# Kernel tuning notes

Hardware: AMD Instinct MI355X
Metric: run time of the kernel (lower is better)

The kernel has to match this reference:

```python
import jax, jax.numpy as jnp
import numpy as np

N_SITES = 64   # lattice sites
BOND = 32      # virtual bond dimension D
PHYS = 2       # physical (spin) dimension
BATCH = 32768  # Monte Carlo samples


def spin_to_occupancy(s):
    # spins in {-1,+1} -> physical indices in {0,1}
    return ((s + 1) // 2).astype(jnp.int32)


def setup_inputs() -> dict:
    key = jax.random.key(0)
    k1, k2, k3, k4 = jax.random.split(key, 4)
    # site tensors: boundary sites have bond dim 1, interior sites are (PHYS, D, D)
    t_first = jax.random.uniform(k1, (PHYS, 1, BOND), dtype=jnp.float32)
    t_mid = jax.random.uniform(k2, (N_SITES - 2, PHYS, BOND, BOND), dtype=jnp.float32)
    t_last = jax.random.uniform(k3, (PHYS, BOND, 1), dtype=jnp.float32)
    bits = jax.random.randint(k4, (BATCH, N_SITES), 0, 2)
    x = (2 * bits - 1).astype(jnp.int32)  # spins +-1
    return {"t_first": t_first, "t_mid": t_mid, "t_last": t_last, "x": x}


def reference(t_first, t_mid, t_last, x):
    idx = spin_to_occupancy(x)  # (B, n_sites)
    # first site: left bond = 1, so state = t_first[idx0, 0, :]  (B, D)
    state = t_first[idx[:, 0], 0, :]

    # interior sites: sequential chain of gather + batched mat-vec
    def step(state, xs):
        T, i = xs            # T: (PHYS, D, D), i: (B,)
        mats = T[i]          # (B, D, D) gather by physical index
        return jnp.einsum('bi,bij->bj', state, mats), None

    state, _ = jax.lax.scan(step, state, (t_mid, idx[:, 1:-1].T))

    # last site: right bond = 1
    amps = jnp.einsum('bi,bi->b', state, t_last[idx[:, -1], :, 0])  # (B,)
    return jnp.log(amps)
```

## Files before the change

kernel.cpp:

```cpp
#include <hip/hip_runtime.h>
#include <math.h>

#define NPAIR 31
#define BATCH 32768

typedef float f32x4 __attribute__((ext_vector_type(4)));
typedef int   i32x8 __attribute__((ext_vector_type(8)));
typedef unsigned int u32x2 __attribute__((ext_vector_type(2)));
typedef unsigned int u32x4 __attribute__((ext_vector_type(4)));

__device__ __forceinline__ unsigned pack_fp8x4(float a, float b, float c, float d) {
    int r = __builtin_amdgcn_cvt_pk_fp8_f32(a, b, 0, false);
    r = __builtin_amdgcn_cvt_pk_fp8_f32(c, d, r, true);
    return (unsigned)r;
}

__device__ __forceinline__ void lane_swap16(unsigned a, unsigned& ev, unsigned& od) {
#if __has_builtin(__builtin_amdgcn_permlane16_swap)
    auto r = __builtin_amdgcn_permlane16_swap((int)a, (int)a, false, false);
    ev = (unsigned)r[0]; od = (unsigned)r[1];
#else
    unsigned p = (unsigned)__shfl_xor((int)a, 16);
    bool hi = (threadIdx.x >> 4) & 1;
    ev = hi ? p : a; od = hi ? a : p;
#endif
}
__device__ __forceinline__ void lane_swap32(unsigned a, unsigned& lo, unsigned& hi) {
#if __has_builtin(__builtin_amdgcn_permlane32_swap)
    auto r = __builtin_amdgcn_permlane32_swap((int)a, (int)a, false, false);
    lo = (unsigned)r[0]; hi = (unsigned)r[1];
#else
    unsigned p = (unsigned)__shfl_xor((int)a, 32);
    bool up = (threadIdx.x & 32) != 0;
    lo = up ? p : a; hi = up ? a : p;
#endif
}

__global__ __launch_bounds__(64) void prefix_kernel(const float* __restrict__ t_mid,
                                                    unsigned* __restrict__ wsP) {
    __shared__ float M1s[1024], M2s[1024];
    const int l = threadIdx.x, h = l >> 4, m = l & 15;
    const int i = blockIdx.x >> 2, v = blockIdx.x & 3;

    const float4* s1 = (const float4*)(t_mid + (size_t)((2 * i) * 2 + (v & 1)) * 1024);
    const float4* s2 = (const float4*)(t_mid + (size_t)((2 * i + 1) * 2 + (v >> 1)) * 1024);
    #pragma unroll
    for (int c = 0; c < 4; ++c) {
        ((float4*)M1s)[c * 64 + l] = s1[c * 64 + l];
        ((float4*)M2s)[c * 64 + l] = s2[c * 64 + l];
    }
    __syncthreads();

    float colv[2][32];
    #pragma unroll
    for (int t = 0; t < 2; ++t)
        #pragma unroll
        for (int mm = 0; mm < 32; ++mm)
            colv[t][mm] = M2s[mm * 32 + 16 * t + m];

    float o0[8], o1[8];
    #pragma unroll
    for (int j = 0; j < 8; ++j) {
        int a = 16 * (j >> 2) + 4 * h + (j & 3);
        float acc0 = 0.f, acc1 = 0.f;
        #pragma unroll
        for (int mm = 0; mm < 32; ++mm) {
            float r = M1s[a * 32 + mm];
            acc0 = fmaf(r, colv[0][mm], acc0);
            acc1 = fmaf(r, colv[1][mm], acc1);
        }
        o0[j] = acc0;
        o1[j] = acc1;
    }

    unsigned* dst0 = wsP + (((size_t)blockIdx.x * 2 + 0) * 16 + m) * 8 + h * 2;
    u32x2 w0 = {pack_fp8x4(o0[0], o0[1], o0[2], o0[3]),
                pack_fp8x4(o0[4], o0[5], o0[6], o0[7])};
    *(u32x2*)dst0 = w0;
    unsigned* dst1 = wsP + (((size_t)blockIdx.x * 2 + 1) * 16 + m) * 8 + h * 2;
    u32x2 w1 = {pack_fp8x4(o1[0], o1[1], o1[2], o1[3]),
                pack_fp8x4(o1[4], o1[5], o1[6], o1[7])};
    *(u32x2*)dst1 = w1;
}

#define MPS_STEP(QQ, PF) do {                                                 \
    unsigned vl = (unsigned)mrot & 3u; mrot >>= 2;                            \
    unsigned E0, O0, E1, O1;                                                  \
    lane_swap16(Bd0, E0, O0); lane_swap16(Bd1, E1, O1);                       \
    unsigned g0, g1, g2, g3, g4, g5, g6, g7;                                  \
    lane_swap32(E0, g0, g4); lane_swap32(E1, g1, g5);                         \
    lane_swap32(O0, g2, g6); lane_swap32(O1, g3, g7);                         \
    bool selq = (vl == (unsigned)q);                                          \
    i32x8 Bv;                                                                 \
    Bv[0] = selq ? (int)g0 : 0; Bv[1] = selq ? (int)g1 : 0;                   \
    Bv[2] = selq ? (int)g2 : 0; Bv[3] = selq ? (int)g3 : 0;                   \
    Bv[4] = selq ? (int)g4 : 0; Bv[5] = selq ? (int)g5 : 0;                   \
    Bv[6] = selq ? (int)g6 : 0; Bv[7] = selq ? (int)g7 : 0;                   \
    i32x8 A0v, A1v;                                                           \
    A0v[0]=(int)QQ[0][0]; A0v[1]=(int)QQ[0][1]; A0v[2]=(int)QQ[0][2]; A0v[3]=(int)QQ[0][3]; \
    A0v[4]=(int)QQ[1][0]; A0v[5]=(int)QQ[1][1]; A0v[6]=(int)QQ[1][2]; A0v[7]=(int)QQ[1][3]; \
    A1v[0]=(int)QQ[2][0]; A1v[1]=(int)QQ[2][1]; A1v[2]=(int)QQ[2][2]; A1v[3]=(int)QQ[2][3]; \
    A1v[4]=(int)QQ[3][0]; A1v[5]=(int)QQ[3][1]; A1v[6]=(int)QQ[3][2]; A1v[7]=(int)QQ[3][3]; \
    const u32x4* pf_ = (PF);                                                  \
    if (pf_) { QQ[0] = pf_[0]; QQ[1] = pf_[1]; QQ[2] = pf_[32]; QQ[3] = pf_[33]; } \
    f32x4 y0 = __builtin_amdgcn_mfma_scale_f32_16x16x128_f8f6f4(              \
        A0v, Bv, cz, 0, 0, 0, 0x7f7f7f7f, 0, 0x7f7f7f7f);                     \
    f32x4 y1 = __builtin_amdgcn_mfma_scale_f32_16x16x128_f8f6f4(              \
        A1v, Bv, cz, 0, 0, 0, 0x7f7f7f7f, 0, 0x7f7f7f7f);                     \
    _Pragma("unroll")                                                         \
    for (int r = 0; r < 4; ++r) { st[r] = y0[r]; st[4 + r] = y1[r]; }         \
    float mx = fmaxf(fmaxf(fmaxf(st[0], st[1]), fmaxf(st[2], st[3])),         \
                     fmaxf(fmaxf(st[4], st[5]), fmaxf(st[6], st[7])));        \
    { unsigned a_, b_;                                                        \
      lane_swap16(__float_as_uint(mx), a_, b_);                               \
      mx = fmaxf(__uint_as_float(a_), __uint_as_float(b_));                   \
      lane_swap32(__float_as_uint(mx), a_, b_);                               \
      mx = fmaxf(__uint_as_float(a_), __uint_as_float(b_)); }                 \
    int ex = (int)((__float_as_uint(mx) >> 23) & 0xFF) - 127;                 \
    float sc = __uint_as_float((unsigned)(127 - ex) << 23);                   \
    _Pragma("unroll")                                                         \
    for (int j = 0; j < 8; ++j) st[j] *= sc;                                  \
    expsum += ex;                                                             \
    Bd0 = pack_fp8x4(st[0], st[1], st[2], st[3]);                             \
    Bd1 = pack_fp8x4(st[4], st[5], st[6], st[7]);                             \
} while (0)

__global__ __launch_bounds__(256, 2) void mps_mfma_kernel(
    const float* __restrict__ t_first,
    const float* __restrict__ t_last,
    const int*   __restrict__ x,
    const unsigned* __restrict__ wsP,
    float* __restrict__ out)
{
    const int tid  = threadIdx.x;
    const int w    = tid >> 6;
    const int l    = tid & 63;
    const int q    = l >> 4;
    const int e    = l & 15;
    const int base = (blockIdx.x * 4 + w) * 16;

    unsigned long long mrot;
    {
        const int4* xr = (const int4*)(x + (size_t)(base + e) * 64 + 16 * q);
        unsigned chunk = 0;
        #pragma unroll
        for (int c = 0; c < 4; ++c) {
            int4 vv = xr[c];
            chunk |= (unsigned)(vv.x > 0) << (4 * c + 0);
            chunk |= (unsigned)(vv.y > 0) << (4 * c + 1);
            chunk |= (unsigned)(vv.z > 0) << (4 * c + 2);
            chunk |= (unsigned)(vv.w > 0) << (4 * c + 3);
        }
        unsigned sh = chunk << ((q & 1) * 16);
        unsigned lo = (q < 2) ? sh : 0u;
        unsigned hi = (q >= 2) ? sh : 0u;
        lo |= (unsigned)__shfl_xor((int)lo, 16);
        lo |= (unsigned)__shfl_xor((int)lo, 32);
        hi |= (unsigned)__shfl_xor((int)hi, 16);
        hi |= (unsigned)__shfl_xor((int)hi, 32);
        unsigned long long mask = ((unsigned long long)hi << 32) | lo;
        mrot = mask >> 1;
    }

    float st[8];
    {
        const float* tf = t_first + ((x[(size_t)(base + e) * 64] > 0) ? 32 : 0);
        #pragma unroll
        for (int j = 0; j < 8; ++j)
            st[j] = tf[16 * (j >> 2) + 4 * q + (j & 3)];
    }
    unsigned Bd0 = pack_fp8x4(st[0], st[1], st[2], st[3]);
    unsigned Bd1 = pack_fp8x4(st[4], st[5], st[6], st[7]);

    int expsum = 0;
    const f32x4 cz = {0.f, 0.f, 0.f, 0.f};

    const u32x4* Wl = (const u32x4*)wsP + (q * 64 + e * 2);
    u32x4 Q0[4], Q1[4];
    Q0[0] = Wl[0];   Q0[1] = Wl[1];   Q0[2] = Wl[32];  Q0[3] = Wl[33];
    Q1[0] = Wl[256]; Q1[1] = Wl[257]; Q1[2] = Wl[288]; Q1[3] = Wl[289];

    const u32x4* pf = Wl + 512;
    for (int k = 0; k < 15; ++k) {
        MPS_STEP(Q0, pf);
        MPS_STEP(Q1, (k < 14) ? (pf + 256) : (const u32x4*)0);
        pf += 512;
    }
    MPS_STEP(Q0, (const u32x4*)0);

    const float* tl = t_last + ((mrot & 1ull) ? 32 : 0);
    float amp = 0.f;
    #pragma unroll
    for (int j = 0; j < 8; ++j)
        amp = fmaf(st[j], tl[16 * (j >> 2) + 4 * q + (j & 3)], amp);
    amp += __shfl_xor(amp, 16);
    amp += __shfl_xor(amp, 32);

    if (l < 16)
        out[base + l] = logf(amp) + 0.69314718055994531f * (float)expsum;
}

extern "C" void kernel_launch(void* const* d_in, const int* in_sizes, int n_in,
                              void* d_out, int out_size, void* d_ws, size_t ws_size,
                              hipStream_t stream) {
    const float* t_first = (const float*)d_in[0];
    const float* t_mid   = (const float*)d_in[1];
    const float* t_last  = (const float*)d_in[2];
    const int*   x       = (const int*)d_in[3];
    float* out           = (float*)d_out;

    unsigned* wsP = (unsigned*)d_ws;

    hipLaunchKernelGGL(prefix_kernel, dim3(NPAIR * 4), dim3(64), 0, stream, t_mid, wsP);
    hipLaunchKernelGGL(mps_mfma_kernel, dim3(BATCH / 64), dim3(256), 0, stream,
                       t_first, t_last, x, wsP, out);
}
```

Baseline: 80.64 us.

## Relayout fp8 pair-product workspace for coalesced loads and deepen prefetch to two steps

The precompute kernel now writes the packed fp8 pair matrices so that each lane's A-fragment for a step sits in contiguous 64-lane rows. The main kernel can then load it with fully coalesced 16-byte loads indexed by lane. The chain loop is fully unrolled with a 4-slot register ring that prefetches two steps ahead instead of one, to hide global load latency behind the MFMA and rescale chain. This costs more VGPRs, which could pressure the 2-waves-per-SIMD launch bound.

```diff
diff --git a/kernel.cpp b/kernel.cpp
--- a/kernel.cpp
+++ b/kernel.cpp
@@ -73,57 +73,16 @@
         o1[j] = acc1;
     }
 
-    unsigned* dst0 = wsP + (((size_t)blockIdx.x * 2 + 0) * 16 + m) * 8 + h * 2;
+    const int slot4 = (v * 16 + m) * 4 + (h & 1) * 2;
+    unsigned* dst0 = wsP + (size_t)(4 * i + (h >> 1)) * 256 + slot4;
     u32x2 w0 = {pack_fp8x4(o0[0], o0[1], o0[2], o0[3]),
                 pack_fp8x4(o0[4], o0[5], o0[6], o0[7])};
     *(u32x2*)dst0 = w0;
-    unsigned* dst1 = wsP + (((size_t)blockIdx.x * 2 + 1) * 16 + m) * 8 + h * 2;
+    unsigned* dst1 = wsP + (size_t)(4 * i + 2 + (h >> 1)) * 256 + slot4;
     u32x2 w1 = {pack_fp8x4(o1[0], o1[1], o1[2], o1[3]),
                 pack_fp8x4(o1[4], o1[5], o1[6], o1[7])};
     *(u32x2*)dst1 = w1;
 }
-
-#define MPS_STEP(QQ, PF) do {                                                 \
-    unsigned vl = (unsigned)mrot & 3u; mrot >>= 2;                            \
-    unsigned E0, O0, E1, O1;                                                  \
-    lane_swap16(Bd0, E0, O0); lane_swap16(Bd1, E1, O1);                       \
-    unsigned g0, g1, g2, g3, g4, g5, g6, g7;                                  \
-    lane_swap32(E0, g0, g4); lane_swap32(E1, g1, g5);                         \
-    lane_swap32(O0, g2, g6); lane_swap32(O1, g3, g7);                         \
-    bool selq = (vl == (unsigned)q);                                          \
-    i32x8 Bv;                                                                 \
-    Bv[0] = selq ? (int)g0 : 0; Bv[1] = selq ? (int)g1 : 0;                   \
-    Bv[2] = selq ? (int)g2 : 0; Bv[3] = selq ? (int)g3 : 0;                   \
-    Bv[4] = selq ? (int)g4 : 0; Bv[5] = selq ? (int)g5 : 0;                   \
-    Bv[6] = selq ? (int)g6 : 0; Bv[7] = selq ? (int)g7 : 0;                   \
-    i32x8 A0v, A1v;                                                           \
-    A0v[0]=(int)QQ[0][0]; A0v[1]=(int)QQ[0][1]; A0v[2]=(int)QQ[0][2]; A0v[3]=(int)QQ[0][3]; \
-    A0v[4]=(int)QQ[1][0]; A0v[5]=(int)QQ[1][1]; A0v[6]=(int)QQ[1][2]; A0v[7]=(int)QQ[1][3]; \
-    A1v[0]=(int)QQ[2][0]; A1v[1]=(int)QQ[2][1]; A1v[2]=(int)QQ[2][2]; A1v[3]=(int)QQ[2][3]; \
-    A1v[4]=(int)QQ[3][0]; A1v[5]=(int)QQ[3][1]; A1v[6]=(int)QQ[3][2]; A1v[7]=(int)QQ[3][3]; \
-    const u32x4* pf_ = (PF);                                                  \
-    if (pf_) { QQ[0] = pf_[0]; QQ[1] = pf_[1]; QQ[2] = pf_[32]; QQ[3] = pf_[33]; } \
-    f32x4 y0 = __builtin_amdgcn_mfma_scale_f32_16x16x128_f8f6f4(              \
-        A0v, Bv, cz, 0, 0, 0, 0x7f7f7f7f, 0, 0x7f7f7f7f);                     \
-    f32x4 y1 = __builtin_amdgcn_mfma_scale_f32_16x16x128_f8f6f4(              \
-        A1v, Bv, cz, 0, 0, 0, 0x7f7f7f7f, 0, 0x7f7f7f7f);                     \
-    _Pragma("unroll")                                                         \
-    for (int r = 0; r < 4; ++r) { st[r] = y0[r]; st[4 + r] = y1[r]; }         \
-    float mx = fmaxf(fmaxf(fmaxf(st[0], st[1]), fmaxf(st[2], st[3])),         \
-                     fmaxf(fmaxf(st[4], st[5]), fmaxf(st[6], st[7])));        \
-    { unsigned a_, b_;                                                        \
-      lane_swap16(__float_as_uint(mx), a_, b_);                               \
-      mx = fmaxf(__uint_as_float(a_), __uint_as_float(b_));                   \
-      lane_swap32(__float_as_uint(mx), a_, b_);                               \
-      mx = fmaxf(__uint_as_float(a_), __uint_as_float(b_)); }                 \
-    int ex = (int)((__float_as_uint(mx) >> 23) & 0xFF) - 127;                 \
-    float sc = __uint_as_float((unsigned)(127 - ex) << 23);                   \
-    _Pragma("unroll")                                                         \
-    for (int j = 0; j < 8; ++j) st[j] *= sc;                                  \
-    expsum += ex;                                                             \
-    Bd0 = pack_fp8x4(st[0], st[1], st[2], st[3]);                             \
-    Bd1 = pack_fp8x4(st[4], st[5], st[6], st[7]);                             \
-} while (0)
 
 __global__ __launch_bounds__(256, 2) void mps_mfma_kernel(
     const float* __restrict__ t_first,
@@ -175,18 +134,71 @@
     int expsum = 0;
     const f32x4 cz = {0.f, 0.f, 0.f, 0.f};
 
-    const u32x4* Wl = (const u32x4*)wsP + (q * 64 + e * 2);
-    u32x4 Q0[4], Q1[4];
-    Q0[0] = Wl[0];   Q0[1] = Wl[1];   Q0[2] = Wl[32];  Q0[3] = Wl[33];
-    Q1[0] = Wl[256]; Q1[1] = Wl[257]; Q1[2] = Wl[288]; Q1[3] = Wl[289];
-
-    const u32x4* pf = Wl + 512;
-    for (int k = 0; k < 15; ++k) {
-        MPS_STEP(Q0, pf);
-        MPS_STEP(Q1, (k < 14) ? (pf + 256) : (const u32x4*)0);
-        pf += 512;
-    }
-    MPS_STEP(Q0, (const u32x4*)0);
+    const u32x4* Wl = (const u32x4*)wsP + l;
+
+    i32x8 Af0[4], Af1[4];
+#define LOADSLOT(sl, ss) do {                         \
+        ((u32x4*)&Af0[sl])[0] = Wl[(4 * (ss) + 0) * 64]; \
+        ((u32x4*)&Af0[sl])[1] = Wl[(4 * (ss) + 1) * 64]; \
+        ((u32x4*)&Af1[sl])[0] = Wl[(4 * (ss) + 2) * 64]; \
+        ((u32x4*)&Af1[sl])[1] = Wl[(4 * (ss) + 3) * 64]; \
+    } while (0)
+
+    LOADSLOT(0, 0);
+    LOADSLOT(1, 1);
+
+    #pragma unroll
+    for (int s = 0; s < 31; ++s) {
+        const int sl = s & 3;
+        unsigned vl = (unsigned)mrot & 3u;
+        mrot >>= 2;
+
+        unsigned E0, O0, E1, O1;
+        lane_swap16(Bd0, E0, O0);
+        lane_swap16(Bd1, E1, O1);
+        unsigned g0, g1, g2, g3, g4, g5, g6, g7;
+        lane_swap32(E0, g0, g4);
+        lane_swap32(E1, g1, g5);
+        lane_swap32(O0, g2, g6);
+        lane_swap32(O1, g3, g7);
+
+        const bool selq = (vl == (unsigned)q);
+        i32x8 Bv;
+        Bv[0] = selq ? (int)g0 : 0; Bv[1] = selq ? (int)g1 : 0;
+        Bv[2] = selq ? (int)g2 : 0; Bv[3] = selq ? (int)g3 : 0;
+        Bv[4] = selq ? (int)g4 : 0; Bv[5] = selq ? (int)g5 : 0;
+        Bv[6] = selq ? (int)g6 : 0; Bv[7] = selq ? (int)g7 : 0;
+
+        if (s < 29) {
+            const int psl = (s + 2) & 3;
+            LOADSLOT(psl, s + 2);
+        }
+
+        f32x4 y0 = __builtin_amdgcn_mfma_scale_f32_16x16x128_f8f6f4(
+            Af0[sl], Bv, cz, 0, 0, 0, 0x7f7f7f7f, 0, 0x7f7f7f7f);
+        f32x4 y1 = __builtin_amdgcn_mfma_scale_f32_16x16x128_f8f6f4(
+            Af1[sl], Bv, cz, 0, 0, 0, 0x7f7f7f7f, 0, 0x7f7f7f7f);
+
+        #pragma unroll
+        for (int r = 0; r < 4; ++r) { st[r] = y0[r]; st[4 + r] = y1[r]; }
+
+        float mx = fmaxf(fmaxf(fmaxf(st[0], st[1]), fmaxf(st[2], st[3])),
+                         fmaxf(fmaxf(st[4], st[5]), fmaxf(st[6], st[7])));
+        unsigned a_, b_;
+        lane_swap16(__float_as_uint(mx), a_, b_);
+        mx = fmaxf(__uint_as_float(a_), __uint_as_float(b_));
+        lane_swap32(__float_as_uint(mx), a_, b_);
+        mx = fmaxf(__uint_as_float(a_), __uint_as_float(b_));
+        int ex = (int)((__float_as_uint(mx) >> 23) & 0xFF) - 127;
+        float sc = __uint_as_float((unsigned)(127 - ex) << 23);
+        #pragma unroll
+        for (int j = 0; j < 8; ++j) st[j] *= sc;
+        expsum += ex;
+
+        Bd0 = pack_fp8x4(st[0], st[1], st[2], st[3]);
+        Bd1 = pack_fp8x4(st[4], st[5], st[6], st[7]);
+    }
+#undef LOADSLOT
 
     const float* tl = t_last + ((mrot & 1ull) ? 32 : 0);
     float amp = 0.f;
```

After: 80.30 us. Within noise of the previous version (-0.4%).
